# Kernel optimization log

Measured on AMD Instinct MI355X. Metric: run time of the kernel, lower is better.

Reference implementation:

```python
import jax, jax.numpy as jnp
import numpy as np

D_MODEL = 1024
D_INNER = 2 * D_MODEL
D_STATE = 16
DT_RANK = (D_MODEL + 15) // 16  # math.ceil(d_model/16) = 64
D_CONV = 4
SEQ_L = 2048
BATCH = 2


def setup_inputs() -> dict:
    key = jax.random.key(0)
    ks = jax.random.split(key, 8)
    def w(k, shape, scale=0.02):
        return jax.random.normal(k, shape, dtype=jnp.float32) * scale
    x = jax.random.normal(ks[0], (SEQ_L, BATCH, D_MODEL), dtype=jnp.float32)
    # weights stored as (in, out); torch Linear is x @ W.T with W (out, in)
    W_in = w(ks[1], (D_MODEL, 2 * D_INNER))
    W_conv = w(ks[2], (D_INNER, 1, D_CONV), 0.3)  # depthwise conv kernel (O, I/groups=1, K)
    b_conv = jnp.zeros((D_INNER,), jnp.float32)
    W_x = w(ks[3], (D_INNER, DT_RANK + 2 * D_STATE))
    W_dt = w(ks[4], (DT_RANK, D_INNER))
    b_dt = jnp.zeros((D_INNER,), jnp.float32)
    A_log = jnp.log(jnp.broadcast_to(jnp.arange(1, D_STATE + 1, dtype=jnp.float32),
                                     (D_INNER, D_STATE)))
    D = jnp.ones((D_INNER,), jnp.float32)
    W_out = w(ks[5], (D_INNER, D_MODEL))
    return {"x": x, "W_in": W_in, "W_conv": W_conv, "b_conv": b_conv,
            "W_x": W_x, "W_dt": W_dt, "b_dt": b_dt,
            "A_log": A_log, "D": D, "W_out": W_out}


def _mamba_forward(x, W_in, W_conv, b_conv, W_x, W_dt, b_dt, A_log, D, W_out):
    xb = jnp.transpose(x, (1, 0, 2))                       # (b, l, d_model)
    b, l, _ = xb.shape
    x_and_res = xb @ W_in                                  # (b, l, 2*d_inner)
    xs, res = jnp.split(x_and_res, 2, axis=-1)
    # depthwise causal conv1d: torch pads d_conv-1 both sides then truncates to l
    xc = jnp.transpose(xs, (0, 2, 1))                      # (b, d_inner, l)
    xc = jax.lax.conv_general_dilated(
        xc, W_conv, window_strides=(1,), padding=[(D_CONV - 1, 0)],
        feature_group_count=D_INNER,
        dimension_numbers=("NCH", "OIH", "NCH")) + b_conv[None, :, None]
    u = jax.nn.silu(jnp.transpose(xc, (0, 2, 1)))          # (b, l, d_inner)
    # SSM parameters
    A = -jnp.exp(A_log)                                    # (d_inner, n)
    x_dbl = u @ W_x                                        # (b, l, dt_rank + 2n)
    delta, Bm, Cm = jnp.split(x_dbl, [DT_RANK, DT_RANK + D_STATE], axis=-1)
    delta = jax.nn.softplus(delta @ W_dt + b_dt)           # (b, l, d_inner)
    # selective scan: state (b, d_inner, n)
    def step(state, inp):
        d_t, B_t, C_t, u_t = inp                           # (b,d_in),(b,n),(b,n),(b,d_in)
        dA = jnp.exp(d_t[:, :, None] * A)                  # (b, d_inner, n)
        dBu = d_t[:, :, None] * B_t[:, None, :] * u_t[:, :, None]
        state = dA * state + dBu
        y_t = jnp.einsum("bdn,bn->bd", state, C_t)
        return state, y_t

    init = jnp.zeros((b, D_INNER, D_STATE), jnp.float32)
    seq = (jnp.moveaxis(delta, 1, 0), jnp.moveaxis(Bm, 1, 0),
           jnp.moveaxis(Cm, 1, 0), jnp.moveaxis(u, 1, 0))
    _, ys = jax.lax.scan(step, init, seq)                  # (l, b, d_inner)
    y = jnp.moveaxis(ys, 0, 1) + u * D                     # (b, l, d_inner)
    y = y * jax.nn.silu(res)
    return y @ W_out                                       # (b, l, d_model)


def reference(x, W_in, W_conv, b_conv, W_x, W_dt, b_dt, A_log, D, W_out):
    return _mamba_forward(x, W_in, W_conv, b_conv, W_x, W_dt, b_dt, A_log, D, W_out)
```

## Files before the change

kernel.cpp:

```cpp
#include <hip/hip_runtime.h>
#include <hip/hip_bf16.h>

#define L_SEQ  2048
#define NBATCH 2
#define DMODEL 1024
#define DINNER 2048
#define DSTATE 16
#define DTRANK 64
#define MROWS  (L_SEQ * NBATCH)
#define NCHUNK 64
#define LCHUNK 32
#define LOG2E  1.44269504f

using bf16 = __hip_bfloat16;
typedef short s16x8 __attribute__((ext_vector_type(8)));
typedef float f32x4 __attribute__((ext_vector_type(4)));

__device__ __forceinline__ void gload_lds16(const bf16* g, bf16* l) {
    __builtin_amdgcn_global_load_lds(
        (const __attribute__((address_space(1))) void*)g,
        (__attribute__((address_space(3))) void*)l, 16, 0, 0);
}

__device__ __forceinline__ float bf2f(short v) {
    return __uint_as_float(((unsigned)(unsigned short)v) << 16);
}

__global__ __launch_bounds__(512, 2)
void gemm256(const bf16* __restrict__ A, const bf16* __restrict__ Bt,
             bf16* __restrict__ C, int N, int K, int lda, int ldb)
{
    __shared__ __align__(16) bf16 As[2][256 * 64];
    __shared__ __align__(16) bf16 Bs[2][256 * 64];

    const int tid  = threadIdx.x;
    const int wid  = tid >> 6;
    const int lane = tid & 63;
    const int wr = wid >> 2, wc = wid & 3;
    const int fr = lane & 15, fk = lane >> 4;

    const int nbx = gridDim.x;
    const int nwg = nbx * gridDim.y;
    int id = blockIdx.y * nbx + blockIdx.x;
    int cpx = nwg >> 3;
    id = (id & 7) * cpx + (id >> 3);
    const long bm = (long)(id / nbx) * 256;
    const long bn = (long)(id % nbx) * 256;

    const int q0 = tid, q1 = tid + 512;
    const int r0 = q0 >> 3, r1 = q1 >> 3;
    const int c0 = ((q0 & 7) ^ (r0 & 7)) << 3;
    const int c1 = ((q1 & 7) ^ (r1 & 7)) << 3;
    const bf16* sA0h0 = A  + (bm + r0)       * (long)lda + c0;
    const bf16* sA1h0 = A  + (bm + r1)       * (long)lda + c1;
    const bf16* sA0h1 = A  + (bm + 128 + r0) * (long)lda + c0;
    const bf16* sA1h1 = A  + (bm + 128 + r1) * (long)lda + c1;
    const bf16* sB0h0 = Bt + (bn + r0)       * (long)ldb + c0;
    const bf16* sB1h0 = Bt + (bn + r1)       * (long)ldb + c1;
    const bf16* sB0h1 = Bt + (bn + 128 + r0) * (long)ldb + c0;
    const bf16* sB1h1 = Bt + (bn + 128 + r1) * (long)ldb + c1;
    const int dst0 = wid * 512;
    const int dst1 = 4096 + wid * 512;

    const int o0   = ((fk ^ (fr & 7)) << 3);
    const int o1   = o0 ^ 32;
    const int rA64 = (wr * 64 + fr) * 64;
    const int rB64 = (wc * 32 + fr) * 64;

    f32x4 acc[8][4] = {};
    s16x8 af[4][2], bf0[2][2], bf1[2][2];
    const int nt = K >> 6;

#define STAGE(ARR, BUF, H, P0, P1) do {                    \
        gload_lds16(P0, &ARR[BUF][(H) * 8192 + dst0]);     \
        gload_lds16(P1, &ARR[BUF][(H) * 8192 + dst1]);     \
        P0 += 64; P1 += 64;                                \
    } while (0)

#define LOADA(MH, CUR) do {                                   \
        const bf16* ab = &As[CUR][rA64 + (MH) * 8192];        \
        _Pragma("unroll") for (int m = 0; m < 4; ++m) {       \
            af[m][0] = *(const s16x8*)&ab[m * 1024 + o0];     \
            af[m][1] = *(const s16x8*)&ab[m * 1024 + o1]; }   \
    } while (0)

#define LOADB(NH, CUR, BF) do {                               \
        const bf16* bb = &Bs[CUR][rB64 + (NH) * 8192];        \
        _Pragma("unroll") for (int n = 0; n < 2; ++n) {       \
            BF[n][0] = *(const s16x8*)&bb[n * 1024 + o0];     \
            BF[n][1] = *(const s16x8*)&bb[n * 1024 + o1]; }   \
    } while (0)

#define MFMAQ(MH, NH, BF) do {                                               \
        __builtin_amdgcn_s_setprio(1);                                       \
        _Pragma("unroll") for (int ks = 0; ks < 2; ++ks)                     \
        _Pragma("unroll") for (int m = 0; m < 4; ++m)                        \
        _Pragma("unroll") for (int n = 0; n < 2; ++n)                        \
            acc[(MH) * 4 + m][(NH) * 2 + n] =                                \
                __builtin_amdgcn_mfma_f32_16x16x32_bf16(                     \
                    af[m][ks], BF[n][ks], acc[(MH) * 4 + m][(NH) * 2 + n],   \
                    0, 0, 0);                                                \
        __builtin_amdgcn_s_setprio(0);                                       \
    } while (0)

#define WB(NV) asm volatile("s_waitcnt vmcnt(" #NV ")\n\ts_barrier" ::: "memory")

    STAGE(As, 0, 0, sA0h0, sA1h0);
    STAGE(Bs, 0, 0, sB0h0, sB1h0);
    STAGE(Bs, 0, 1, sB0h1, sB1h1);
    STAGE(As, 0, 1, sA0h1, sA1h1);
    WB(4);

    int cur = 0;
    for (int t = 0; t < nt - 1; ++t) {
        STAGE(As, cur ^ 1, 0, sA0h0, sA1h0);
        STAGE(Bs, cur ^ 1, 0, sB0h0, sB1h0);
        STAGE(Bs, cur ^ 1, 1, sB0h1, sB1h1);
        STAGE(As, cur ^ 1, 1, sA0h1, sA1h1);
        LOADA(0, cur); LOADB(0, cur, bf0);
        MFMAQ(0, 0, bf0);  WB(10);
        LOADB(1, cur, bf1);
        MFMAQ(0, 1, bf1);  WB(8);
        LOADA(1, cur);
        MFMAQ(1, 1, bf1);
        MFMAQ(1, 0, bf0);  WB(4);
        cur ^= 1;
    }
    LOADA(0, cur); LOADB(0, cur, bf0);
    MFMAQ(0, 0, bf0);  WB(2);
    LOADB(1, cur, bf1);
    MFMAQ(0, 1, bf1);  WB(0);
    LOADA(1, cur);
    MFMAQ(1, 1, bf1);
    MFMAQ(1, 0, bf0);

#undef STAGE
#undef LOADA
#undef LOADB
#undef MFMAQ
#undef WB

    #pragma unroll
    for (int mh = 0; mh < 2; ++mh)
    #pragma unroll
    for (int m = 0; m < 4; ++m)
    #pragma unroll
    for (int nh = 0; nh < 2; ++nh)
    #pragma unroll
    for (int n = 0; n < 2; ++n) {
        f32x4 v = acc[mh * 4 + m][nh * 2 + n];
        long row0 = bm + wr * 64 + mh * 128 + m * 16 + fk * 4;
        long col  = bn + wc * 32 + nh * 128 + n * 16 + fr;
        #pragma unroll
        for (int j = 0; j < 4; ++j)
            C[(row0 + j) * N + col] = __float2bfloat16(v[j]);
    }
}

template<typename OutT, int EPI, bool SPLITK = false>
__global__ __launch_bounds__(256)
void gemm_bt(const bf16* __restrict__ A, const bf16* __restrict__ Bt,
             OutT* __restrict__ C, const float* __restrict__ bias,
             int M, int N, int K, int lda, int ldb)
{
    __shared__ __align__(16) bf16 As[2][128 * 32];
    __shared__ __align__(16) bf16 Bs[2][128 * 32];

    const int tid  = threadIdx.x;
    const int wave = tid >> 6;
    const int lane = tid & 63;
    const int wr = wave >> 1, wc = wave & 1;
    const int fr = lane & 15, fk = lane >> 4;

    const int nbx = gridDim.x;
    const int nwg = nbx * gridDim.y;
    int id  = blockIdx.y * nbx + blockIdx.x;
    if (nwg >= 8) {
        int cpx = nwg >> 3;
        id = (id & 7) * cpx + (id >> 3);
    }
    const int bxi = id % nbx, byi = id / nbx;
    const long bm = (long)byi * 128;
    const long bn = (long)bxi * 128;

    if constexpr (SPLITK) {
        long ko = (long)blockIdx.z * K;
        A  += ko;
        Bt += ko;
        C  += (size_t)blockIdx.z * M * N;
    }

    const int r0 = tid >> 2,         c0 = (tid & 3) << 3;
    const int r1 = (256 + tid) >> 2, c1 = c0;
    const bf16* pA0 = A  + (bm + r0) * (long)lda + c0;
    const bf16* pA1 = A  + (bm + r1) * (long)lda + c1;
    const bf16* pB0 = Bt + (bn + r0) * (long)ldb + c0;
    const bf16* pB1 = Bt + (bn + r1) * (long)ldb + c1;
    const size_t ld0 = (size_t)(wave * 64) * 8;
    const size_t ld1 = (size_t)(256 + wave * 64) * 8;

    f32x4 acc[4][4] = {};
    const int nt = K >> 5;

    gload_lds16(pA0, &As[0][ld0]);
    gload_lds16(pB0, &Bs[0][ld0]);
    gload_lds16(pA1, &As[0][ld1]);
    gload_lds16(pB1, &Bs[0][ld1]);
    pA0 += 32; pA1 += 32; pB0 += 32; pB1 += 32;
    __syncthreads();

    int cur = 0;
    for (int t = 0; t < nt; ++t) {
        if (t + 1 < nt) {
            gload_lds16(pA0, &As[cur ^ 1][ld0]);
            gload_lds16(pB0, &Bs[cur ^ 1][ld0]);
            gload_lds16(pA1, &As[cur ^ 1][ld1]);
            gload_lds16(pB1, &Bs[cur ^ 1][ld1]);
            pA0 += 32; pA1 += 32; pB0 += 32; pB1 += 32;
        }

        s16x8 afrag[4], bfrag[4];
        #pragma unroll
        for (int m = 0; m < 4; ++m)
            afrag[m] = *(const s16x8*)&As[cur][(wr * 64 + m * 16 + fr) * 32 + fk * 8];
        #pragma unroll
        for (int n = 0; n < 4; ++n)
            bfrag[n] = *(const s16x8*)&Bs[cur][(wc * 64 + n * 16 + fr) * 32 + fk * 8];

        #pragma unroll
        for (int m = 0; m < 4; ++m)
            #pragma unroll
            for (int n = 0; n < 4; ++n)
                acc[m][n] = __builtin_amdgcn_mfma_f32_16x16x32_bf16(
                    afrag[m], bfrag[n], acc[m][n], 0, 0, 0);

        __syncthreads();
        cur ^= 1;
    }

    #pragma unroll
    for (int m = 0; m < 4; ++m)
        #pragma unroll
        for (int n = 0; n < 4; ++n) {
            f32x4 v = acc[m][n];
            long row0 = bm + wr * 64 + m * 16 + fk * 4;
            long col  = bn + wc * 64 + n * 16 + fr;
            #pragma unroll
            for (int j = 0; j < 4; ++j) {
                float val = v[j];
                if (EPI == 1) {
                    val += bias[col];
                    val = (val > 20.f) ? val : log1pf(__expf(val));
                }
                if constexpr (sizeof(OutT) == 2)
                    C[(row0 + j) * N + col] = __float2bfloat16(val);
                else
                    C[(row0 + j) * N + col] = val;
            }
        }
}

__global__ void transpose_bf16(const float* __restrict__ in, bf16* __restrict__ out,
                               int R, int C, int Cpad)
{
    __shared__ float tile[32][33];
    int cb = blockIdx.x * 32, rb = blockIdx.y * 32;
    int tx = threadIdx.x, ty = threadIdx.y;
    #pragma unroll
    for (int i = 0; i < 4; ++i) {
        int r = rb + ty + i * 8, c = cb + tx;
        tile[ty + i * 8][tx] = (r < R && c < C) ? in[(long)r * C + c] : 0.f;
    }
    __syncthreads();
    #pragma unroll
    for (int i = 0; i < 4; ++i) {
        int oc = cb + ty + i * 8;
        int orow = rb + tx;
        if (oc < Cpad && orow < R)
            out[(long)oc * R + orow] = __float2bfloat16(tile[tx][ty + i * 8]);
    }
}

__global__ void convert_x_kernel(const float* __restrict__ x, bf16* __restrict__ Xb)
{
    int idx = blockIdx.x * 256 + threadIdx.x;
    int c   = idx & (DMODEL - 1);
    int row = idx >> 10;
    int l   = row & (L_SEQ - 1);
    int b   = row >> 11;
    Xb[idx] = __float2bfloat16(x[((l * NBATCH + b) << 10) | c]);
}

__global__ void conv_silu_kernel(const bf16* __restrict__ xr, const float* __restrict__ Wc,
                                 const float* __restrict__ bc, bf16* __restrict__ u)
{
    int idx = blockIdx.x * 256 + threadIdx.x;
    int g   = idx & 255;
    int row = idx >> 8;
    int c   = g << 3;
    int l   = row & (L_SEQ - 1);

    float acc[8];
    f32x4 bi0 = *(const f32x4*)(bc + c);
    f32x4 bi1 = *(const f32x4*)(bc + c + 4);
    #pragma unroll
    for (int j = 0; j < 4; ++j) { acc[j] = bi0[j]; acc[4 + j] = bi1[j]; }

    f32x4 w[8];
    #pragma unroll
    for (int j = 0; j < 8; ++j) w[j] = *(const f32x4*)(Wc + (c + j) * 4);

    #pragma unroll
    for (int t = 0; t < 4; ++t) {
        int ll = l - 3 + t;
        if (ll >= 0) {
            s16x8 v = *(const s16x8*)(xr + (long)(row - 3 + t) * 4096 + c);
            #pragma unroll
            for (int j = 0; j < 8; ++j)
                acc[j] += bf2f(v[j]) * w[j][t];
        }
    }
    s16x8 o;
    #pragma unroll
    for (int j = 0; j < 8; ++j) {
        float a = acc[j];
        float s = a / (1.f + __builtin_amdgcn_exp2f(-LOG2E * a));
        bf16 h = __float2bfloat16(s);
        o[j] = *(short*)&h;
    }
    *(s16x8*)(u + (long)row * DINNER + c) = o;
}

__global__ void reduce_xdbl(const float* __restrict__ part, float* __restrict__ xdbl,
                            bf16* __restrict__ drbf)
{
    int idx = blockIdx.x * 256 + threadIdx.x;
    const size_t stride = (size_t)MROWS * 128;
    float v = part[idx] + part[idx + stride] + part[idx + 2 * stride]
            + part[idx + 3 * stride];
    xdbl[idx] = v;
    int col = idx & 127;
    if (col < 64)
        drbf[(idx >> 7) * 64 + col] = __float2bfloat16(v);
}

__global__ void reduce_out(const float* __restrict__ part, float* __restrict__ out)
{
    int i = blockIdx.x * 256 + threadIdx.x;
    f32x4 a = ((const f32x4*)part)[i];
    f32x4 b = ((const f32x4*)(part + (size_t)MROWS * DMODEL))[i];
    ((f32x4*)out)[i] = a + b;
}

__global__ __launch_bounds__(256)
void scan_phase1(const bf16* __restrict__ delta, const bf16* __restrict__ u,
                 const float* __restrict__ xdbl, const float* __restrict__ A_log,
                 float* __restrict__ AS)
{
    const int idx   = blockIdx.x * 256 + threadIdx.x;
    const int half  = idx & 1;
    const int ch    = idx >> 1;
    const int chunk = blockIdx.y;
    const int d     = ch & (DINNER - 1);
    const int b     = ch >> 11;
    const int n0    = half * 8;

    float A2[8], s[8];
    const f32x4* Arow = (const f32x4*)(A_log + d * DSTATE + n0);
    #pragma unroll
    for (int q = 0; q < 2; ++q) {
        f32x4 v = Arow[q];
        #pragma unroll
        for (int j = 0; j < 4; ++j) A2[q * 4 + j] = -__expf(v[j]) * LOG2E;
    }
    #pragma unroll
    for (int n = 0; n < 8; ++n) s[n] = 0.f;
    float sdl = 0.f;

    bool fastA = true;
    #pragma unroll
    for (int j = 0; j < 8; ++j)
        fastA &= fabsf(A2[j] + (float)(n0 + j + 1) * LOG2E)
                 < 0.01f * (float)(n0 + j + 1);

    const long row0 = (long)b * L_SEQ + chunk * LCHUNK;
    const bf16*  pD = delta + row0 * DINNER + d;
    const bf16*  pU = u     + row0 * DINNER + d;
    const f32x4* pB = (const f32x4*)(xdbl + row0 * 128 + 64 + n0);

    if (fastA) {
        #pragma unroll 4
        for (int l = 0; l < LCHUNK; ++l) {
            float dl = __bfloat162float(*pD);
            float uv = __bfloat162float(*pU);
            f32x4 B0 = pB[0], B1 = pB[1];
            pD += DINNER; pU += DINNER; pB += 32;
            float dbu = dl * uv;
            sdl += dl;
            float b1 = __builtin_amdgcn_exp2f(-LOG2E * dl);
            float b2 = b1 * b1, b3 = b2 * b1, b4 = b2 * b2;
            float b5 = b4 * b1, b6 = b4 * b2, b7 = b4 * b3, b8 = b4 * b4;
            float pre = half ? b8 : 1.f;
            s[0] = pre * b1 * s[0] + dbu * B0[0];
            s[1] = pre * b2 * s[1] + dbu * B0[1];
            s[2] = pre * b3 * s[2] + dbu * B0[2];
            s[3] = pre * b4 * s[3] + dbu * B0[3];
            s[4] = pre * b5 * s[4] + dbu * B1[0];
            s[5] = pre * b6 * s[5] + dbu * B1[1];
            s[6] = pre * b7 * s[6] + dbu * B1[2];
            s[7] = pre * b8 * s[7] + dbu * B1[3];
        }
    } else {
        #pragma unroll 4
        for (int l = 0; l < LCHUNK; ++l) {
            float dl = __bfloat162float(*pD);
            float uv = __bfloat162float(*pU);
            f32x4 B0 = pB[0], B1 = pB[1];
            pD += DINNER; pU += DINNER; pB += 32;
            float dbu = dl * uv;
            sdl += dl;
            #pragma unroll
            for (int j = 0; j < 4; ++j) {
                float e = __builtin_amdgcn_exp2f(dl * A2[j]);
                s[j] = e * s[j] + dbu * B0[j];
            }
            #pragma unroll
            for (int j = 0; j < 4; ++j) {
                float e = __builtin_amdgcn_exp2f(dl * A2[4 + j]);
                s[4 + j] = e * s[4 + j] + dbu * B1[j];
            }
        }
    }
    float ap[8];
    #pragma unroll
    for (int n = 0; n < 8; ++n) ap[n] = __builtin_amdgcn_exp2f(sdl * A2[n]);

    float* o = AS + ((size_t)chunk * 4096 + ch) * 32 + n0;
    *(f32x4*)(o)      = *(f32x4*)&ap[0];
    *(f32x4*)(o + 4)  = *(f32x4*)&ap[4];
    *(f32x4*)(o + 16) = *(f32x4*)&s[0];
    *(f32x4*)(o + 20) = *(f32x4*)&s[4];
}

__global__ __launch_bounds__(256)
void scan_phase2(float* __restrict__ AS)
{
    const int idx = blockIdx.x * 256 + threadIdx.x;
    const int n   = idx & 15;
    const int ch  = idx >> 4;

    float s = 0.f;
    for (int cb = 0; cb < NCHUNK; cb += 16) {
        float av[16], sv[16];
        #pragma unroll
        for (int j = 0; j < 16; ++j) {
            size_t r = ((size_t)(cb + j) * 4096 + ch) * 32 + n;
            av[j] = AS[r];
            sv[j] = AS[r + 16];
        }
        #pragma unroll
        for (int j = 0; j < 16; ++j) {
            AS[((size_t)(cb + j) * 4096 + ch) * 32 + 16 + n] = s;
            s = av[j] * s + sv[j];
        }
    }
}

__global__ __launch_bounds__(256)
void scan_phase3(const bf16* __restrict__ delta, const bf16* __restrict__ u,
                 const float* __restrict__ xdbl, const bf16* __restrict__ xr,
                 const float* __restrict__ AS, const float* __restrict__ A_log,
                 const float* __restrict__ Dp, bf16* __restrict__ ybf)
{
    const int idx   = blockIdx.x * 256 + threadIdx.x;
    const int half  = idx & 1;
    const int ch    = idx >> 1;
    const int chunk = blockIdx.y;
    const int d     = ch & (DINNER - 1);
    const int b     = ch >> 11;
    const int n0    = half * 8;

    float A2[8], s[8];
    const f32x4* Arow = (const f32x4*)(A_log + d * DSTATE + n0);
    #pragma unroll
    for (int q = 0; q < 2; ++q) {
        f32x4 v = Arow[q];
        #pragma unroll
        for (int j = 0; j < 4; ++j) A2[q * 4 + j] = -__expf(v[j]) * LOG2E;
    }
    const float* ip = AS + ((size_t)chunk * 4096 + ch) * 32 + 16 + n0;
    *(f32x4*)&s[0] = *(const f32x4*)(ip);
    *(f32x4*)&s[4] = *(const f32x4*)(ip + 4);

    bool fastA = true;
    #pragma unroll
    for (int j = 0; j < 8; ++j)
        fastA &= fabsf(A2[j] + (float)(n0 + j + 1) * LOG2E)
                 < 0.01f * (float)(n0 + j + 1);

    const float Dd  = Dp[d];
    const long row0 = (long)b * L_SEQ + chunk * LCHUNK;

    const bf16*  pD = delta + row0 * DINNER + d;
    const bf16*  pU = u     + row0 * DINNER + d;
    const bf16*  pR = xr    + row0 * 4096 + 2048 + d;
    const f32x4* pB = (const f32x4*)(xdbl + row0 * 128 + 64 + n0);
    bf16*        pY = ybf   + row0 * DINNER + d;

    if (fastA) {
        #pragma unroll 4
        for (int l = 0; l < LCHUNK; ++l) {
            float dl = __bfloat162float(*pD);
            float uv = __bfloat162float(*pU);
            float rs = __bfloat162float(*pR);
            f32x4 B0 = pB[0], B1 = pB[1];
            f32x4 C0 = pB[4], C1 = pB[5];
            pD += DINNER; pU += DINNER; pR += 4096; pB += 32;
            float dbu = dl * uv;
            float b1 = __builtin_amdgcn_exp2f(-LOG2E * dl);
            float b2 = b1 * b1, b3 = b2 * b1, b4 = b2 * b2;
            float b5 = b4 * b1, b6 = b4 * b2, b7 = b4 * b3, b8 = b4 * b4;
            float pre = half ? b8 : 1.f;
            float y0 = 0.f, y1 = 0.f;
            s[0] = pre * b1 * s[0] + dbu * B0[0];  y0 += s[0] * C0[0];
            s[1] = pre * b2 * s[1] + dbu * B0[1];  y0 += s[1] * C0[1];
            s[2] = pre * b3 * s[2] + dbu * B0[2];  y0 += s[2] * C0[2];
            s[3] = pre * b4 * s[3] + dbu * B0[3];  y0 += s[3] * C0[3];
            s[4] = pre * b5 * s[4] + dbu * B1[0];  y1 += s[4] * C1[0];
            s[5] = pre * b6 * s[5] + dbu * B1[1];  y1 += s[5] * C1[1];
            s[6] = pre * b7 * s[6] + dbu * B1[2];  y1 += s[6] * C1[2];
            s[7] = pre * b8 * s[7] + dbu * B1[3];  y1 += s[7] * C1[3];
            float yh = y0 + y1;
            float yt = yh + __shfl_xor(yh, 1);
            if (half == 0) {
                float yf = yt + uv * Dd;
                yf *= rs / (1.f + __builtin_amdgcn_exp2f(-LOG2E * rs));
                *pY = __float2bfloat16(yf);
            }
            pY += DINNER;
        }
    } else {
        #pragma unroll 4
        for (int l = 0; l < LCHUNK; ++l) {
            float dl = __bfloat162float(*pD);
            float uv = __bfloat162float(*pU);
            float rs = __bfloat162float(*pR);
            f32x4 B0 = pB[0], B1 = pB[1];
            f32x4 C0 = pB[4], C1 = pB[5];
            pD += DINNER; pU += DINNER; pR += 4096; pB += 32;
            float dbu = dl * uv;
            float y0 = 0.f, y1 = 0.f;
            #pragma unroll
            for (int j = 0; j < 4; ++j) {
                float e = __builtin_amdgcn_exp2f(dl * A2[j]);
                s[j] = e * s[j] + dbu * B0[j];
                y0 += s[j] * C0[j];
            }
            #pragma unroll
            for (int j = 0; j < 4; ++j) {
                float e = __builtin_amdgcn_exp2f(dl * A2[4 + j]);
                s[4 + j] = e * s[4 + j] + dbu * B1[j];
                y1 += s[4 + j] * C1[j];
            }
            float yh = y0 + y1;
            float yt = yh + __shfl_xor(yh, 1);
            if (half == 0) {
                float yf = yt + uv * Dd;
                yf *= rs / (1.f + __builtin_amdgcn_exp2f(-LOG2E * rs));
                *pY = __float2bfloat16(yf);
            }
            pY += DINNER;
        }
    }
}

extern "C" void kernel_launch(void* const* d_in, const int* in_sizes, int n_in,
                              void* d_out, int out_size, void* d_ws, size_t ws_size,
                              hipStream_t stream)
{
    const float* x      = (const float*)d_in[0];
    const float* W_in   = (const float*)d_in[1];
    const float* W_conv = (const float*)d_in[2];
    const float* b_conv = (const float*)d_in[3];
    const float* W_x    = (const float*)d_in[4];
    const float* W_dt   = (const float*)d_in[5];
    const float* b_dt   = (const float*)d_in[6];
    const float* A_log  = (const float*)d_in[7];
    const float* Dp     = (const float*)d_in[8];
    const float* W_out  = (const float*)d_in[9];
    float* out = (float*)d_out;

    char* ws = (char*)d_ws;
    size_t off = 0;
    auto alloc = [&](size_t bytes) {
        void* p = ws + off;
        off = (off + bytes + 255) & ~(size_t)255;
        return p;
    };
    bf16*  Xb    = (bf16*) alloc((size_t)MROWS * DMODEL * 2);
    bf16*  WinT  = (bf16*) alloc((size_t)4096  * DMODEL * 2);
    bf16*  xr    = (bf16*) alloc((size_t)MROWS * 4096  * 2);
    bf16*  ubf   = (bf16*) alloc((size_t)MROWS * DINNER * 2);
    bf16*  WxT   = (bf16*) alloc((size_t)128   * DINNER * 2);
    float* xdbl  = (float*)alloc((size_t)MROWS * 128 * 4);
    float* xdblp = (float*)alloc((size_t)4 * MROWS * 128 * 4);
    bf16*  drbf  = (bf16*) alloc((size_t)MROWS * 64 * 2);
    bf16*  WdtT  = (bf16*) alloc((size_t)DINNER * 64 * 2);
    bf16*  delta = (bf16*) alloc((size_t)MROWS * DINNER * 2);
    bf16*  ybf   = (bf16*) alloc((size_t)MROWS * DINNER * 2);
    bf16*  WoutT = (bf16*) alloc((size_t)DMODEL * DINNER * 2);
    float* AS    = (float*)alloc((size_t)NCHUNK * 4096 * 32 * 4);

    dim3 tb(32, 8);
    transpose_bf16<<<dim3(128, 32), tb, 0, stream>>>(W_in,  WinT,  1024, 4096, 4096);
    transpose_bf16<<<dim3(4, 64),   tb, 0, stream>>>(W_x,   WxT,   2048, 96,   128);
    transpose_bf16<<<dim3(64, 2),   tb, 0, stream>>>(W_dt,  WdtT,  64,   2048, 2048);
    transpose_bf16<<<dim3(32, 64),  tb, 0, stream>>>(W_out, WoutT, 2048, 1024, 1024);
    convert_x_kernel<<<(MROWS * DMODEL) / 256, 256, 0, stream>>>(x, Xb);

    gemm256<<<dim3(4096 / 256, MROWS / 256), 512, 0, stream>>>(
        Xb, WinT, xr, 4096, 1024, 1024, 1024);
    conv_silu_kernel<<<(MROWS * DINNER / 8) / 256, 256, 0, stream>>>(
        xr, W_conv, b_conv, ubf);
    gemm_bt<float, 0, true><<<dim3(1, MROWS / 128, 4), 256, 0, stream>>>(
        ubf, WxT, xdblp, nullptr, MROWS, 128, 512, 2048, 2048);
    reduce_xdbl<<<(MROWS * 128) / 256, 256, 0, stream>>>(xdblp, xdbl, drbf);
    gemm_bt<bf16, 1><<<dim3(DINNER / 128, MROWS / 128), 256, 0, stream>>>(
        drbf, WdtT, delta, b_dt, MROWS, DINNER, 64, 64, 64);
    scan_phase1<<<dim3(32, NCHUNK), 256, 0, stream>>>(delta, ubf, xdbl, A_log, AS);
    scan_phase2<<<256, 256, 0, stream>>>(AS);
    scan_phase3<<<dim3(32, NCHUNK), 256, 0, stream>>>(delta, ubf, xdbl, xr, AS,
                                                      A_log, Dp, ybf);
    gemm_bt<float, 0, true><<<dim3(DMODEL / 128, MROWS / 128, 2), 256, 0, stream>>>(
        ybf, WoutT, (float*)AS, nullptr, MROWS, DMODEL, 1024, 2048, 2048);
    reduce_out<<<(MROWS * DMODEL) / 1024, 256, 0, stream>>>((float*)AS, out);
}
```

Before: 271.9 us.

## Merge weight transposes and input conversion into one prep launch; remap GEMM tiles per XCD

The four weight-transpose launches and the x-to-bf16 conversion now run as a single kernel that dispatches work by block index, removing four launches and the gaps between them. The large input GEMM's block-to-tile mapping is rewritten so the blocks sharing an XCD cover a compact 4x8 region of output tiles, meant to improve L2 reuse of A and B panels. The new mapping hardcodes the 16x16 grid shape.

```diff
diff --git a/kernel.cpp b/kernel.cpp
--- a/kernel.cpp
+++ b/kernel.cpp
@@ -39,13 +39,12 @@
     const int wr = wid >> 2, wc = wid & 3;
     const int fr = lane & 15, fk = lane >> 4;
 
-    const int nbx = gridDim.x;
-    const int nwg = nbx * gridDim.y;
-    int id = blockIdx.y * nbx + blockIdx.x;
-    int cpx = nwg >> 3;
-    id = (id & 7) * cpx + (id >> 3);
-    const long bm = (long)(id / nbx) * 256;
-    const long bn = (long)(id % nbx) * 256;
+    const int orig = blockIdx.y * gridDim.x + blockIdx.x;
+    const int xcd  = orig & 7, k = orig >> 3;
+    const int byi  = (xcd >> 1) * 4 + (k >> 3);
+    const int bxi  = (xcd & 1) * 8 + (k & 7);
+    const long bm = (long)byi * 256;
+    const long bn = (long)bxi * 256;
 
     const int q0 = tid, q1 = tid + 512;
     const int r0 = q0 >> 3, r1 = q1 >> 3;
@@ -260,12 +259,12 @@
         }
 }
 
-__global__ void transpose_bf16(const float* __restrict__ in, bf16* __restrict__ out,
-                               int R, int C, int Cpad)
+__device__ __forceinline__ void do_transpose(
+    const float* __restrict__ in, bf16* __restrict__ out,
+    int R, int C, int Cpad, int bx, int by, int tx, int ty)
 {
     __shared__ float tile[32][33];
-    int cb = blockIdx.x * 32, rb = blockIdx.y * 32;
-    int tx = threadIdx.x, ty = threadIdx.y;
+    int cb = bx * 32, rb = by * 32;
     #pragma unroll
     for (int i = 0; i < 4; ++i) {
         int r = rb + ty + i * 8, c = cb + tx;
@@ -281,14 +280,36 @@
     }
 }
 
-__global__ void convert_x_kernel(const float* __restrict__ x, bf16* __restrict__ Xb)
-{
-    int idx = blockIdx.x * 256 + threadIdx.x;
-    int c   = idx & (DMODEL - 1);
-    int row = idx >> 10;
-    int l   = row & (L_SEQ - 1);
-    int b   = row >> 11;
-    Xb[idx] = __float2bfloat16(x[((l * NBATCH + b) << 10) | c]);
+__global__ __launch_bounds__(256)
+void prep_kernel(const float* __restrict__ W_in,  bf16* __restrict__ WinT,
+                 const float* __restrict__ W_x,   bf16* __restrict__ WxT,
+                 const float* __restrict__ W_dt,  bf16* __restrict__ WdtT,
+                 const float* __restrict__ W_out, bf16* __restrict__ WoutT,
+                 const float* __restrict__ x,     bf16* __restrict__ Xb)
+{
+    const int b  = blockIdx.x;
+    const int t  = threadIdx.x;
+    const int tx = t & 31, ty = t >> 5;
+
+    if (b < 4096) {
+        do_transpose(W_in, WinT, 1024, 4096, 4096, b & 127, b >> 7, tx, ty);
+    } else if (b < 4352) {
+        int b2 = b - 4096;
+        do_transpose(W_x, WxT, 2048, 96, 128, b2 & 3, b2 >> 2, tx, ty);
+    } else if (b < 4480) {
+        int b3 = b - 4352;
+        do_transpose(W_dt, WdtT, 64, 2048, 2048, b3 & 63, b3 >> 6, tx, ty);
+    } else if (b < 6528) {
+        int b4 = b - 4480;
+        do_transpose(W_out, WoutT, 2048, 1024, 1024, b4 & 31, b4 >> 5, tx, ty);
+    } else {
+        int idx = (b - 6528) * 256 + t;
+        int c   = idx & (DMODEL - 1);
+        int row = idx >> 10;
+        int l   = row & (L_SEQ - 1);
+        int bb  = row >> 11;
+        Xb[idx] = __float2bfloat16(x[((l * NBATCH + bb) << 10) | c]);
+    }
 }
 
 __global__ void conv_silu_kernel(const bf16* __restrict__ xr, const float* __restrict__ Wc,
@@ -611,12 +632,8 @@
     bf16*  WoutT = (bf16*) alloc((size_t)DMODEL * DINNER * 2);
     float* AS    = (float*)alloc((size_t)NCHUNK * 4096 * 32 * 4);
 
-    dim3 tb(32, 8);
-    transpose_bf16<<<dim3(128, 32), tb, 0, stream>>>(W_in,  WinT,  1024, 4096, 4096);
-    transpose_bf16<<<dim3(4, 64),   tb, 0, stream>>>(W_x,   WxT,   2048, 96,   128);
-    transpose_bf16<<<dim3(64, 2),   tb, 0, stream>>>(W_dt,  WdtT,  64,   2048, 2048);
-    transpose_bf16<<<dim3(32, 64),  tb, 0, stream>>>(W_out, WoutT, 2048, 1024, 1024);
-    convert_x_kernel<<<(MROWS * DMODEL) / 256, 256, 0, stream>>>(x, Xb);
+    prep_kernel<<<6528 + (MROWS * DMODEL) / 256, 256, 0, stream>>>(
+        W_in, WinT, W_x, WxT, W_dt, WdtT, W_out, WoutT, x, Xb);
 
     gemm256<<<dim3(4096 / 256, MROWS / 256), 512, 0, stream>>>(
         Xb, WinT, xr, 4096, 1024, 1024, 1024);
```

Result: faster. 263.1 us (-3.2%).
